# Performance work log

Measured on AMD Instinct MI355X. Metric: run time of the kernel, lower is better.

Reference implementation:

```python
import jax, jax.numpy as jnp
import numpy as np

ENC = 768
DEC = 768
B, T, S = 16, 1024, 1024


def setup_inputs() -> dict:
    key = jax.random.key(0)
    k1, k2, k3 = jax.random.split(key, 3)
    inputs = jax.random.normal(k1, (B, T, DEC), dtype=jnp.float32)
    context = jax.random.normal(k2, (B, S, ENC), dtype=jnp.float32)
    # linear_out: Linear(dec+enc -> dec) with bias; torch weight layout [out, in]
    W_out = jax.random.normal(k3, (DEC, DEC + ENC), dtype=jnp.float32) * 0.02
    b_out = jnp.zeros((DEC,), dtype=jnp.float32)
    w_scale = jnp.ones((1, 1, 1), dtype=jnp.float32)   # self.weight
    b_scale = jnp.ones((1, 1, 1), dtype=jnp.float32)   # self.bias
    prelu_a = jnp.full((1,), 0.25, dtype=jnp.float32)  # PReLU single param
    return {"inputs": inputs, "context": context, "W_out": W_out,
            "b_out": b_out, "w_scale": w_scale, "b_scale": b_scale,
            "prelu_a": prelu_a}


def reference(inputs, context, W_out, b_out, w_scale, b_scale, prelu_a):
    # score: bmm(h_t, h_s^T). NOTE: linear_in output is discarded in the
    # original (h_t reassigned), so the raw inputs are used — faithful here.
    align = jnp.einsum('btd,bsd->bts', inputs, context)        # [B,T,S]
    av = jax.nn.softmax(align, axis=-1)                        # softmax over src
    # gate: sigmoid of per-source column-sum over target positions
    gate = jax.nn.sigmoid(jnp.sum(av, axis=1, keepdims=True))  # [B,1,S]
    # AdaptiveAvgPool1d(1): mean over last (src) dim -> [B,T,1]
    pooled = jnp.mean(av, axis=-1, keepdims=True)
    av_g = av * gate * pooled                                  # fused elementwise
    c = jnp.einsum('bts,bsd->btd', av_g, context)              # [B,T,ENC]
    c = c * w_scale + b_scale                                  # scalar affine
    concat_c = jnp.concatenate([c, inputs], axis=-1)           # [B,T,ENC+DEC]
    h = jnp.einsum('btk,dk->btd', concat_c, W_out) + b_out     # linear_out
    attn_h = jnp.where(h >= 0, h, prelu_a * h)                 # PReLU
    return attn_h.transpose(1, 0, 2), av_g.transpose(1, 0, 2)
```

## Files before the change

### kernel.cpp

```cpp
#include <hip/hip_runtime.h>

#define B_ 16
#define T_ 1024
#define S_ 1024
#define D_ 768
#define K3_ 1536
#define BS_ (B_ * S_)
#define BD_ (B_ * D_)
#define NI_ (B_ * T_ * D_)
#define NW_ (D_ * K3_)

typedef __attribute__((ext_vector_type(8))) _Float16 half8;
typedef __attribute__((ext_vector_type(4))) float float4v;

__device__ __forceinline__ unsigned short f2h(float x) {
    return __builtin_bit_cast(unsigned short, (_Float16)x);
}
__device__ __forceinline__ float h2f(unsigned short u) {
    return (float)__builtin_bit_cast(_Float16, u);
}
__device__ __forceinline__ unsigned pkh2(float a, float b) {
    return (unsigned)f2h(a) | ((unsigned)f2h(b) << 16);
}
__device__ __forceinline__ uint2 pkh4(const float4 v) {
    return make_uint2(pkh2(v.x, v.y), pkh2(v.z, v.w));
}

__device__ __forceinline__ void gl_lds16(const void* g, void* l) {
    __builtin_amdgcn_global_load_lds(
        (const __attribute__((address_space(1))) unsigned int*)g,
        (__attribute__((address_space(3))) unsigned int*)l,
        16, 0, 0);
}

#define MFMA_PROLOG() \
    const int tid  = threadIdx.x; \
    const int w    = tid >> 6; \
    const int wm   = (w >> 1) * 64; \
    const int wn   = (w & 1) * 64; \
    const int lane = tid & 63; \
    const int q    = lane >> 4; \
    const int lr   = lane & 15; \
    float4v acc[4][4] = {};

#define STAGE_PROLOG() \
    const int rl0 = (w << 5) + (lane >> 2); \
    const int cc  = (lane & 3) * 8; \
    const int wb  = w * 1024;

#define MFMA_COMPUTE_F16(AS, BS) \
    { \
        half8 afr[4], bfr[4]; \
        _Pragma("unroll") \
        for (int i = 0; i < 4; i++) \
            afr[i] = *(const half8*)&(AS)[(wm + i * 16 + lr) * 32 + q * 8]; \
        _Pragma("unroll") \
        for (int j = 0; j < 4; j++) \
            bfr[j] = *(const half8*)&(BS)[(wn + j * 16 + lr) * 32 + q * 8]; \
        _Pragma("unroll") \
        for (int i = 0; i < 4; i++) \
            _Pragma("unroll") \
            for (int j = 0; j < 4; j++) \
                acc[i][j] = __builtin_amdgcn_mfma_f32_16x16x32_f16( \
                    afr[i], bfr[j], acc[i][j], 0, 0, 0); \
    }

__global__ __launch_bounds__(256) void prep_all(
    const float* __restrict__ ctx, const float* __restrict__ inp,
    const float* __restrict__ W,
    unsigned short* __restrict__ ctxT, unsigned short* __restrict__ ctx_h,
    unsigned short* __restrict__ inp_h, unsigned short* __restrict__ W_h)
{
    __shared__ unsigned short Ts[64 * 68];
    const int bid = blockIdx.x;
    const int tid = threadIdx.x;
    if (bid < 3072) {
        const int b   = bid / 192;
        const int rem = bid - b * 192;
        const int d0  = (rem >> 4) * 64;
        const int s0  = (rem & 15) * 64;
        const int srel = tid >> 4;
        const int dcol = (tid & 15) * 4;
#pragma unroll
        for (int r = 0; r < 4; r++) {
            const int s = srel + r * 16;
            float4 v = *(const float4*)(ctx + ((size_t)b * S_ + s0 + s) * D_ + d0 + dcol);
            Ts[(dcol + 0) * 68 + s] = f2h(v.x);
            Ts[(dcol + 1) * 68 + s] = f2h(v.y);
            Ts[(dcol + 2) * 68 + s] = f2h(v.z);
            Ts[(dcol + 3) * 68 + s] = f2h(v.w);
            *(uint2*)(ctx_h + ((size_t)b * S_ + s0 + s) * D_ + d0 + dcol) = pkh4(v);
        }
        __syncthreads();
        const int drow = tid >> 2;
        const int scg  = (tid & 3) * 16;
        unsigned short* dst = ctxT + ((size_t)b * D_ + d0 + drow) * S_ + s0 + scg;
#pragma unroll
        for (int p = 0; p < 4; p++) {
            uint2 u = *(const uint2*)&Ts[drow * 68 + scg + p * 4];
            *(uint2*)(dst + p * 4) = u;
        }
    } else {
        const size_t i4 = (size_t)(bid - 3072) * 256 + tid;
        const size_t flat = i4 * 4;
        float4 v;
        unsigned short* dst;
        if (flat < NI_) {
            v = ((const float4*)inp)[i4];
            dst = inp_h + flat;
        } else {
            v = *(const float4*)(W + (flat - NI_));
            dst = W_h + (flat - NI_);
        }
        *(uint2*)dst = pkh4(v);
    }
}

__global__ __launch_bounds__(256) void gemm_scores_f16(
    const unsigned short* __restrict__ ctx_h,
    const unsigned short* __restrict__ inp_h,
    float* __restrict__ out2)
{
    const int hwid = blockIdx.x + (blockIdx.y << 3) + (blockIdx.z << 6);
    const int wk   = (hwid & 7) * 128 + (hwid >> 3);
    const int b  = wk >> 6;
    const int t0 = ((wk >> 3) & 7) * 128;
    const int s0 = (wk & 7) * 128;

    __shared__ __align__(16) unsigned short As[2][128 * 32];
    __shared__ __align__(16) unsigned short Bs[2][128 * 32];

    MFMA_PROLOG();
    STAGE_PROLOG();

    const unsigned short* ga0 = ctx_h + ((size_t)b * S_ + s0 + rl0) * D_ + cc;
    const unsigned short* ga1 = ga0 + (size_t)16 * D_;
    const unsigned short* gb0 = inp_h + ((size_t)b * T_ + t0 + rl0) * D_ + cc;
    const unsigned short* gb1 = gb0 + (size_t)16 * D_;

    gl_lds16(ga0, &As[0][wb]);
    gl_lds16(ga1, &As[0][wb + 512]);
    gl_lds16(gb0, &Bs[0][wb]);
    gl_lds16(gb1, &Bs[0][wb + 512]);
    __syncthreads();

    int cur = 0;
    for (int kb = 32; kb < D_; kb += 32) {
        const int nxt = cur ^ 1;
        gl_lds16(ga0 + kb, &As[nxt][wb]);
        gl_lds16(ga1 + kb, &As[nxt][wb + 512]);
        gl_lds16(gb0 + kb, &Bs[nxt][wb]);
        gl_lds16(gb1 + kb, &Bs[nxt][wb + 512]);
        MFMA_COMPUTE_F16(As[cur], Bs[cur]);
        __syncthreads();
        cur = nxt;
    }
    MFMA_COMPUTE_F16(As[cur], Bs[cur]);

#pragma unroll
    for (int i = 0; i < 4; i++)
#pragma unroll
        for (int j = 0; j < 4; j++) {
            const int t = t0 + wn + j * 16 + lr;
            const int s = s0 + wm + i * 16 + q * 4;
            *(float4v*)(out2 + (size_t)t * BS_ + (size_t)b * S_ + s) = acc[i][j];
        }
}

__global__ __launch_bounds__(256) void softmax_rows(
    const float* __restrict__ scores, unsigned short* __restrict__ av_h)
{
    const int bid = blockIdx.x;
    const int b = bid & (B_ - 1);
    const int t = bid / B_;
    const float* row = scores + (size_t)t * BS_ + (size_t)b * S_;
    const int tid = threadIdx.x;

    float4 v = ((const float4*)row)[tid];
    float m = fmaxf(fmaxf(v.x, v.y), fmaxf(v.z, v.w));
#pragma unroll
    for (int off = 32; off > 0; off >>= 1) m = fmaxf(m, __shfl_xor(m, off));

    __shared__ float red[8];
    if ((tid & 63) == 0) red[tid >> 6] = m;
    __syncthreads();
    m = fmaxf(fmaxf(red[0], red[1]), fmaxf(red[2], red[3]));

    float4 e;
    e.x = __expf(v.x - m); e.y = __expf(v.y - m);
    e.z = __expf(v.z - m); e.w = __expf(v.w - m);
    float s = e.x + e.y + e.z + e.w;
#pragma unroll
    for (int off = 32; off > 0; off >>= 1) s += __shfl_xor(s, off);
    if ((tid & 63) == 0) red[4 + (tid >> 6)] = s;
    __syncthreads();
    s = (red[4] + red[5]) + (red[6] + red[7]);

    const float inv = 1.0f / s;
    e.x *= inv; e.y *= inv; e.z *= inv; e.w *= inv;
    unsigned short* orow = av_h + (size_t)t * BS_ + (size_t)b * S_;
    *(uint2*)(orow + tid * 4) = pkh4(e);
}

__global__ __launch_bounds__(256) void colsum_part(
    const unsigned short* __restrict__ av_h, float* __restrict__ partial)
{
    const int b = blockIdx.y;
    const int c = blockIdx.z;
    const int s2 = blockIdx.x * 512 + threadIdx.x * 2;
    const unsigned short* p = av_h + (size_t)(c * 128) * BS_ + (size_t)b * S_ + s2;
    float s0 = 0.0f, s1 = 0.0f;
#pragma unroll 8
    for (int t = 0; t < 128; t++) {
        const unsigned u = *(const unsigned*)(p + (size_t)t * BS_);
        s0 += h2f((unsigned short)(u & 0xffff));
        s1 += h2f((unsigned short)(u >> 16));
    }
    *(float2*)(partial + ((size_t)c * B_ + b) * S_ + s2) = make_float2(s0, s1);
}

__global__ __launch_bounds__(256) void gate_final(
    const float* __restrict__ partial, float* __restrict__ gate)
{
    const int idx = blockIdx.x * 256 + threadIdx.x;
    const int b = idx >> 10, s = idx & (S_ - 1);
    float sum = 0.0f;
#pragma unroll
    for (int c = 0; c < T_ / 128; c++) sum += partial[((size_t)c * B_ + b) * S_ + s];
    gate[idx] = 1.0f / (1.0f + __expf(-sum));
}

__global__ __launch_bounds__(256) void av_out(
    unsigned short* __restrict__ av_h, const float* __restrict__ gate,
    float* __restrict__ out2)
{
    const size_t i8 = ((size_t)blockIdx.x * 256 + threadIdx.x) * 8;
    const int s = (int)(i8 & (S_ - 1));
    const int b = (int)((i8 >> 10) & (B_ - 1));
    const uint4 u = *(const uint4*)(av_h + i8);
    const float4 g0 = *(const float4*)(gate + b * S_ + s);
    const float4 g1 = *(const float4*)(gate + b * S_ + s + 4);
    float a0 = h2f(u.x & 0xffff) * g0.x, a1 = h2f(u.x >> 16) * g0.y;
    float a2 = h2f(u.y & 0xffff) * g0.z, a3 = h2f(u.y >> 16) * g0.w;
    float a4 = h2f(u.z & 0xffff) * g1.x, a5 = h2f(u.z >> 16) * g1.y;
    float a6 = h2f(u.w & 0xffff) * g1.z, a7 = h2f(u.w >> 16) * g1.w;
    const float is = 1.0f / (float)S_;
    *(float4*)(out2 + i8)     = make_float4(a0 * is, a1 * is, a2 * is, a3 * is);
    *(float4*)(out2 + i8 + 4) = make_float4(a4 * is, a5 * is, a6 * is, a7 * is);
    uint4 o;
    o.x = pkh2(a0, a1); o.y = pkh2(a2, a3);
    o.z = pkh2(a4, a5); o.w = pkh2(a6, a7);
    *(uint4*)(av_h + i8) = o;
}

__global__ __launch_bounds__(256) void gemm_ctx_f16(
    const unsigned short* __restrict__ ctxT, const unsigned short* __restrict__ av_h,
    const float* __restrict__ w_scale, const float* __restrict__ b_scale,
    unsigned short* __restrict__ c_h)
{
    const int hwid = blockIdx.x + blockIdx.y * 8 + blockIdx.z * 48;
    const int wk   = (hwid & 7) * 96 + (hwid >> 3);
    const int t0 = (wk % 8) * 128;
    const int d0 = ((wk / 8) % 6) * 128;
    const int b  = wk / 48;

    __shared__ __align__(16) unsigned short As[2][128 * 32];
    __shared__ __align__(16) unsigned short Bs[2][128 * 32];

    MFMA_PROLOG();
    STAGE_PROLOG();

    const unsigned short* ga0 = ctxT + ((size_t)b * D_ + d0 + rl0) * S_ + cc;
    const unsigned short* ga1 = ga0 + (size_t)16 * S_;
    const unsigned short* gb0 = av_h + (size_t)(t0 + rl0) * BS_ + (size_t)b * S_ + cc;
    const unsigned short* gb1 = gb0 + (size_t)16 * BS_;

    gl_lds16(ga0, &As[0][wb]);
    gl_lds16(ga1, &As[0][wb + 512]);
    gl_lds16(gb0, &Bs[0][wb]);
    gl_lds16(gb1, &Bs[0][wb + 512]);
    __syncthreads();

    int cur = 0;
    for (int sb = 32; sb < S_; sb += 32) {
        const int nxt = cur ^ 1;
        gl_lds16(ga0 + sb, &As[nxt][wb]);
        gl_lds16(ga1 + sb, &As[nxt][wb + 512]);
        gl_lds16(gb0 + sb, &Bs[nxt][wb]);
        gl_lds16(gb1 + sb, &Bs[nxt][wb + 512]);
        MFMA_COMPUTE_F16(As[cur], Bs[cur]);
        __syncthreads();
        cur = nxt;
    }
    MFMA_COMPUTE_F16(As[cur], Bs[cur]);

    const float wsc = w_scale[0] * (1.0f / (float)S_);
    const float bsc = b_scale[0];
#pragma unroll
    for (int i = 0; i < 4; i++)
#pragma unroll
        for (int j = 0; j < 4; j++) {
            const int d = d0 + wm + i * 16 + q * 4;
            const int t = t0 + wn + j * 16 + lr;
            uint2 o;
            o.x = pkh2(acc[i][j][0] * wsc + bsc, acc[i][j][1] * wsc + bsc);
            o.y = pkh2(acc[i][j][2] * wsc + bsc, acc[i][j][3] * wsc + bsc);
            *(uint2*)(c_h + ((size_t)b * T_ + t) * D_ + d) = o;
        }
}

__global__ __launch_bounds__(256) void gemm_out_f16(
    const unsigned short* __restrict__ c_h, const unsigned short* __restrict__ inp_h,
    const unsigned short* __restrict__ W_h, const float* __restrict__ bias,
    const float* __restrict__ prelu_a, float* __restrict__ out0)
{
    const int hwid = blockIdx.x + blockIdx.y * 6;
    const int wk   = (hwid & 7) * 96 + (hwid >> 3);
    const int d0 = (wk % 6) * 128;
    const int n0 = (wk / 6) * 128;

    __shared__ __align__(16) unsigned short As[2][128 * 32];
    __shared__ __align__(16) unsigned short Bs[2][128 * 32];

    MFMA_PROLOG();
    STAGE_PROLOG();

    const unsigned short* ga0  = W_h + (size_t)(d0 + rl0) * K3_ + cc;
    const unsigned short* ga1  = ga0 + (size_t)16 * K3_;
    const unsigned short* gbc0 = c_h + (size_t)(n0 + rl0) * D_ + cc;
    const unsigned short* gbi0 = inp_h + (size_t)(n0 + rl0) * D_ + cc;

    gl_lds16(ga0, &As[0][wb]);
    gl_lds16(ga1, &As[0][wb + 512]);
    gl_lds16(gbc0, &Bs[0][wb]);
    gl_lds16(gbc0 + (size_t)16 * D_, &Bs[0][wb + 512]);
    __syncthreads();

    int cur = 0;
    for (int kb = 32; kb < K3_; kb += 32) {
        const int nxt = cur ^ 1;
        const unsigned short* gb0 = (kb < D_) ? gbc0 + kb : gbi0 + (kb - D_);
        gl_lds16(ga0 + kb, &As[nxt][wb]);
        gl_lds16(ga1 + kb, &As[nxt][wb + 512]);
        gl_lds16(gb0, &Bs[nxt][wb]);
        gl_lds16(gb0 + (size_t)16 * D_, &Bs[nxt][wb + 512]);
        MFMA_COMPUTE_F16(As[cur], Bs[cur]);
        __syncthreads();
        cur = nxt;
    }
    MFMA_COMPUTE_F16(As[cur], Bs[cur]);

    const float pa = prelu_a[0];
#pragma unroll
    for (int i = 0; i < 4; i++) {
        const int d = d0 + wm + i * 16 + q * 4;
        const float4 bz = *(const float4*)(bias + d);
#pragma unroll
        for (int j = 0; j < 4; j++) {
            const int n = n0 + wn + j * 16 + lr;
            const int bb = n >> 10;
            const int t = n & (T_ - 1);
            float4 h;
            h.x = acc[i][j][0] + bz.x;
            h.y = acc[i][j][1] + bz.y;
            h.z = acc[i][j][2] + bz.z;
            h.w = acc[i][j][3] + bz.w;
            h.x = h.x >= 0.0f ? h.x : pa * h.x;
            h.y = h.y >= 0.0f ? h.y : pa * h.y;
            h.z = h.z >= 0.0f ? h.z : pa * h.z;
            h.w = h.w >= 0.0f ? h.w : pa * h.w;
            *(float4*)(out0 + (size_t)t * BD_ + (size_t)bb * D_ + d) = h;
        }
    }
}

extern "C" void kernel_launch(void* const* d_in, const int* in_sizes, int n_in,
                              void* d_out, int out_size, void* d_ws, size_t ws_size,
                              hipStream_t stream)
{
    const float* inputs  = (const float*)d_in[0];
    const float* context = (const float*)d_in[1];
    const float* W_out   = (const float*)d_in[2];
    const float* b_out   = (const float*)d_in[3];
    const float* w_scale = (const float*)d_in[4];
    const float* b_scale = (const float*)d_in[5];
    const float* prelu_a = (const float*)d_in[6];

    float* out0 = (float*)d_out;
    float* out2 = out0 + (size_t)T_ * B_ * D_;

    unsigned short* c_h   = (unsigned short*)d_ws;
    unsigned short* ctxT  = c_h   + (size_t)B_ * T_ * D_;
    unsigned short* av_h  = ctxT  + (size_t)B_ * D_ * S_;
    unsigned short* inp_h = av_h  + (size_t)T_ * B_ * S_;
    unsigned short* W_h   = inp_h + (size_t)B_ * T_ * D_;
    float* gate    = (float*)(W_h + (size_t)NW_);
    float* partial = gate + (size_t)B_ * S_;

    prep_all<<<3072 + (NI_ + NW_) / 4 / 256, 256, 0, stream>>>(
        context, inputs, W_out, ctxT, c_h, inp_h, W_h);
    gemm_scores_f16<<<dim3(S_ / 128, T_ / 128, B_), 256, 0, stream>>>(
        c_h , inp_h, out2);
    softmax_rows<<<B_ * T_, 256, 0, stream>>>(out2, av_h);
    colsum_part<<<dim3(S_ / 512, B_, T_ / 128), 256, 0, stream>>>(av_h, partial);
    gate_final<<<(B_ * S_) / 256, 256, 0, stream>>>(partial, gate);
    av_out<<<(int)(((size_t)T_ * B_ * S_ / 8) / 256), 256, 0, stream>>>(
        av_h, gate, out2);
    gemm_ctx_f16<<<dim3(T_ / 128, D_ / 128, B_), 256, 0, stream>>>(
        ctxT, av_h, w_scale, b_scale, c_h);
    gemm_out_f16<<<dim3(D_ / 128, (B_ * T_) / 128), 256, 0, stream>>>(
        c_h, inp_h, W_h, b_out, prelu_a, out0);
}
```

Before: 384.1 us.

## Use triple-buffered LDS pipeline with explicit vmcnt waits and XOR-swizzled tiles

The three MFMA GEMM kernels move from a double-buffered loop with __syncthreads to a three-stage LDS ring, where loads run two tiles ahead and explicit s_waitcnt vmcnt counts plus s_barrier gate each compute step. The global-to-LDS column offset and the fragment read offset are XOR-swizzled to spread LDS accesses across banks. The goal is to hide global load latency and cut LDS bank conflicts. The cost is 50% more shared memory per block, which may lower occupancy, and the hand-written wait counts depend on each stage issuing exactly four loads.

```diff
diff --git a/kernel.cpp b/kernel.cpp
--- a/kernel.cpp
+++ b/kernel.cpp
@@ -45,24 +45,51 @@
 
 #define STAGE_PROLOG() \
     const int rl0 = (w << 5) + (lane >> 2); \
-    const int cc  = (lane & 3) * 8; \
-    const int wb  = w * 1024;
-
-#define MFMA_COMPUTE_F16(AS, BS) \
+    const int cc  = ((lane & 3) ^ ((lane >> 3) & 3)) * 8; \
+    const int wb  = w * 1024; \
+    const int qa  = (q ^ ((lr >> 1) & 3)) * 8;
+
+#define MFMA_COMPUTE_F16(AP, BP) \
     { \
         half8 afr[4], bfr[4]; \
         _Pragma("unroll") \
         for (int i = 0; i < 4; i++) \
-            afr[i] = *(const half8*)&(AS)[(wm + i * 16 + lr) * 32 + q * 8]; \
+            afr[i] = *(const half8*)&(AP)[(wm + i * 16 + lr) * 32 + qa]; \
         _Pragma("unroll") \
         for (int j = 0; j < 4; j++) \
-            bfr[j] = *(const half8*)&(BS)[(wn + j * 16 + lr) * 32 + q * 8]; \
+            bfr[j] = *(const half8*)&(BP)[(wn + j * 16 + lr) * 32 + qa]; \
         _Pragma("unroll") \
         for (int i = 0; i < 4; i++) \
             _Pragma("unroll") \
             for (int j = 0; j < 4; j++) \
                 acc[i][j] = __builtin_amdgcn_mfma_f32_16x16x32_f16( \
                     afr[i], bfr[j], acc[i][j], 0, 0, 0); \
+    }
+
+#define PIPE3_LOOP(NT, STAGE) \
+    STAGE(0, 0); \
+    STAGE(1, 1); \
+    { \
+        int cb = 0; \
+        for (int t = 0; t < (NT); ++t) { \
+            if (t + 2 < (NT)) { \
+                const int sb3 = (cb == 0) ? 2 : cb - 1; \
+                STAGE(sb3, t + 2); \
+            } \
+            if (t < (NT) - 2) { \
+                asm volatile("s_waitcnt vmcnt(8)" ::: "memory"); \
+            } else if (t == (NT) - 2) { \
+                asm volatile("s_waitcnt vmcnt(4)" ::: "memory"); \
+            } else { \
+                asm volatile("s_waitcnt vmcnt(0)" ::: "memory"); \
+            } \
+            __builtin_amdgcn_s_barrier(); \
+            __builtin_amdgcn_sched_barrier(0); \
+            MFMA_COMPUTE_F16(&As[cb * 4096], &Bs[cb * 4096]); \
+            __builtin_amdgcn_sched_barrier(0); \
+            __builtin_amdgcn_s_barrier(); \
+            cb = (cb == 2) ? 0 : cb + 1; \
+        } \
     }
 
 __global__ __launch_bounds__(256) void prep_all(
@@ -127,8 +154,8 @@
     const int t0 = ((wk >> 3) & 7) * 128;
     const int s0 = (wk & 7) * 128;
 
-    __shared__ __align__(16) unsigned short As[2][128 * 32];
-    __shared__ __align__(16) unsigned short Bs[2][128 * 32];
+    __shared__ __align__(16) unsigned short As[3 * 128 * 32];
+    __shared__ __align__(16) unsigned short Bs[3 * 128 * 32];
 
     MFMA_PROLOG();
     STAGE_PROLOG();
@@ -138,24 +165,16 @@
     const unsigned short* gb0 = inp_h + ((size_t)b * T_ + t0 + rl0) * D_ + cc;
     const unsigned short* gb1 = gb0 + (size_t)16 * D_;
 
-    gl_lds16(ga0, &As[0][wb]);
-    gl_lds16(ga1, &As[0][wb + 512]);
-    gl_lds16(gb0, &Bs[0][wb]);
-    gl_lds16(gb1, &Bs[0][wb + 512]);
-    __syncthreads();
-
-    int cur = 0;
-    for (int kb = 32; kb < D_; kb += 32) {
-        const int nxt = cur ^ 1;
-        gl_lds16(ga0 + kb, &As[nxt][wb]);
-        gl_lds16(ga1 + kb, &As[nxt][wb + 512]);
-        gl_lds16(gb0 + kb, &Bs[nxt][wb]);
-        gl_lds16(gb1 + kb, &Bs[nxt][wb + 512]);
-        MFMA_COMPUTE_F16(As[cur], Bs[cur]);
-        __syncthreads();
-        cur = nxt;
-    }
-    MFMA_COMPUTE_F16(As[cur], Bs[cur]);
+#define STAGE_G1(bi, tt) \
+    { \
+        const int kb = (tt) * 32; \
+        gl_lds16(ga0 + kb, &As[(bi) * 4096 + wb]); \
+        gl_lds16(ga1 + kb, &As[(bi) * 4096 + wb + 512]); \
+        gl_lds16(gb0 + kb, &Bs[(bi) * 4096 + wb]); \
+        gl_lds16(gb1 + kb, &Bs[(bi) * 4096 + wb + 512]); \
+    }
+
+    PIPE3_LOOP(D_ / 32, STAGE_G1);
 
 #pragma unroll
     for (int i = 0; i < 4; i++)
@@ -264,8 +283,8 @@
     const int d0 = ((wk / 8) % 6) * 128;
     const int b  = wk / 48;
 
-    __shared__ __align__(16) unsigned short As[2][128 * 32];
-    __shared__ __align__(16) unsigned short Bs[2][128 * 32];
+    __shared__ __align__(16) unsigned short As[3 * 128 * 32];
+    __shared__ __align__(16) unsigned short Bs[3 * 128 * 32];
 
     MFMA_PROLOG();
     STAGE_PROLOG();
@@ -275,24 +294,16 @@
     const unsigned short* gb0 = av_h + (size_t)(t0 + rl0) * BS_ + (size_t)b * S_ + cc;
     const unsigned short* gb1 = gb0 + (size_t)16 * BS_;
 
-    gl_lds16(ga0, &As[0][wb]);
-    gl_lds16(ga1, &As[0][wb + 512]);
-    gl_lds16(gb0, &Bs[0][wb]);
-    gl_lds16(gb1, &Bs[0][wb + 512]);
-    __syncthreads();
-
-    int cur = 0;
-    for (int sb = 32; sb < S_; sb += 32) {
-        const int nxt = cur ^ 1;
-        gl_lds16(ga0 + sb, &As[nxt][wb]);
-        gl_lds16(ga1 + sb, &As[nxt][wb + 512]);
-        gl_lds16(gb0 + sb, &Bs[nxt][wb]);
-        gl_lds16(gb1 + sb, &Bs[nxt][wb + 512]);
-        MFMA_COMPUTE_F16(As[cur], Bs[cur]);
-        __syncthreads();
-        cur = nxt;
-    }
-    MFMA_COMPUTE_F16(As[cur], Bs[cur]);
+#define STAGE_G2(bi, tt) \
+    { \
+        const int sbk = (tt) * 32; \
+        gl_lds16(ga0 + sbk, &As[(bi) * 4096 + wb]); \
+        gl_lds16(ga1 + sbk, &As[(bi) * 4096 + wb + 512]); \
+        gl_lds16(gb0 + sbk, &Bs[(bi) * 4096 + wb]); \
+        gl_lds16(gb1 + sbk, &Bs[(bi) * 4096 + wb + 512]); \
+    }
+
+    PIPE3_LOOP(S_ / 32, STAGE_G2);
 
     const float wsc = w_scale[0] * (1.0f / (float)S_);
     const float bsc = b_scale[0];
@@ -319,8 +330,8 @@
     const int d0 = (wk % 6) * 128;
     const int n0 = (wk / 6) * 128;
 
-    __shared__ __align__(16) unsigned short As[2][128 * 32];
-    __shared__ __align__(16) unsigned short Bs[2][128 * 32];
+    __shared__ __align__(16) unsigned short As[3 * 128 * 32];
+    __shared__ __align__(16) unsigned short Bs[3 * 128 * 32];
 
     MFMA_PROLOG();
     STAGE_PROLOG();
@@ -330,25 +341,17 @@
     const unsigned short* gbc0 = c_h + (size_t)(n0 + rl0) * D_ + cc;
     const unsigned short* gbi0 = inp_h + (size_t)(n0 + rl0) * D_ + cc;
 
-    gl_lds16(ga0, &As[0][wb]);
-    gl_lds16(ga1, &As[0][wb + 512]);
-    gl_lds16(gbc0, &Bs[0][wb]);
-    gl_lds16(gbc0 + (size_t)16 * D_, &Bs[0][wb + 512]);
-    __syncthreads();
-
-    int cur = 0;
-    for (int kb = 32; kb < K3_; kb += 32) {
-        const int nxt = cur ^ 1;
-        const unsigned short* gb0 = (kb < D_) ? gbc0 + kb : gbi0 + (kb - D_);
-        gl_lds16(ga0 + kb, &As[nxt][wb]);
-        gl_lds16(ga1 + kb, &As[nxt][wb + 512]);
-        gl_lds16(gb0, &Bs[nxt][wb]);
-        gl_lds16(gb0 + (size_t)16 * D_, &Bs[nxt][wb + 512]);
-        MFMA_COMPUTE_F16(As[cur], Bs[cur]);
-        __syncthreads();
-        cur = nxt;
-    }
-    MFMA_COMPUTE_F16(As[cur], Bs[cur]);
+#define STAGE_G3(bi, tt) \
+    { \
+        const int kb = (tt) * 32; \
+        const unsigned short* gbx = (kb < D_) ? gbc0 + kb : gbi0 + (kb - D_); \
+        gl_lds16(ga0 + kb, &As[(bi) * 4096 + wb]); \
+        gl_lds16(ga1 + kb, &As[(bi) * 4096 + wb + 512]); \
+        gl_lds16(gbx, &Bs[(bi) * 4096 + wb]); \
+        gl_lds16(gbx + (size_t)16 * D_, &Bs[(bi) * 4096 + wb + 512]); \
+    }
+
+    PIPE3_LOOP(K3_ / 32, STAGE_G3);
 
     const float pa = prelu_a[0];
 #pragma unroll
```

Result: slower. 393.3 us (+2.4%).

## Store scores in fp16 in place and XOR-swizzle LDS tiles for MFMA reads

Applied to the files above, without the earlier changes.

The score GEMM now writes fp16 scores into the av_h buffer instead of fp32 into the output, and softmax reads and writes that buffer in place. This halves the traffic for the intermediate score matrix (written once, read once). Separately, the LDS staging column and the fragment read offset are XOR-swizzled by row bits to reduce bank conflicts on the half8 reads in all three GEMMs. Rounding scores to fp16 before softmax loses precision in the logits, which with unit-normal inputs over 768 dims can be large in magnitude.

```diff
diff --git a/kernel.cpp b/kernel.cpp
--- a/kernel.cpp
+++ b/kernel.cpp
@@ -45,18 +45,19 @@
 
 #define STAGE_PROLOG() \
     const int rl0 = (w << 5) + (lane >> 2); \
-    const int cc  = (lane & 3) * 8; \
-    const int wb  = w * 1024;
-
-#define MFMA_COMPUTE_F16(AS, BS) \
+    const int cc  = ((lane & 3) ^ ((lane >> 3) & 3)) * 8; \
+    const int wb  = w * 1024; \
+    const int qa  = (q ^ ((lr >> 1) & 3)) * 8;
+
+#define MFMA_COMPUTE_F16(AP, BP) \
     { \
         half8 afr[4], bfr[4]; \
         _Pragma("unroll") \
         for (int i = 0; i < 4; i++) \
-            afr[i] = *(const half8*)&(AS)[(wm + i * 16 + lr) * 32 + q * 8]; \
+            afr[i] = *(const half8*)&(AP)[(wm + i * 16 + lr) * 32 + qa]; \
         _Pragma("unroll") \
         for (int j = 0; j < 4; j++) \
-            bfr[j] = *(const half8*)&(BS)[(wn + j * 16 + lr) * 32 + q * 8]; \
+            bfr[j] = *(const half8*)&(BP)[(wn + j * 16 + lr) * 32 + qa]; \
         _Pragma("unroll") \
         for (int i = 0; i < 4; i++) \
             _Pragma("unroll") \
@@ -119,7 +120,7 @@
 __global__ __launch_bounds__(256) void gemm_scores_f16(
     const unsigned short* __restrict__ ctx_h,
     const unsigned short* __restrict__ inp_h,
-    float* __restrict__ out2)
+    unsigned short* __restrict__ sc_h)
 {
     const int hwid = blockIdx.x + (blockIdx.y << 3) + (blockIdx.z << 6);
     const int wk   = (hwid & 7) * 128 + (hwid >> 3);
@@ -127,8 +128,8 @@
     const int t0 = ((wk >> 3) & 7) * 128;
     const int s0 = (wk & 7) * 128;
 
-    __shared__ __align__(16) unsigned short As[2][128 * 32];
-    __shared__ __align__(16) unsigned short Bs[2][128 * 32];
+    __shared__ __align__(16) unsigned short As[2 * 128 * 32];
+    __shared__ __align__(16) unsigned short Bs[2 * 128 * 32];
 
     MFMA_PROLOG();
     STAGE_PROLOG();
@@ -138,24 +139,25 @@
     const unsigned short* gb0 = inp_h + ((size_t)b * T_ + t0 + rl0) * D_ + cc;
     const unsigned short* gb1 = gb0 + (size_t)16 * D_;
 
-    gl_lds16(ga0, &As[0][wb]);
-    gl_lds16(ga1, &As[0][wb + 512]);
-    gl_lds16(gb0, &Bs[0][wb]);
-    gl_lds16(gb1, &Bs[0][wb + 512]);
+#define STAGE_G1(bi, kb) \
+    { \
+        gl_lds16(ga0 + (kb), &As[(bi) * 4096 + wb]); \
+        gl_lds16(ga1 + (kb), &As[(bi) * 4096 + wb + 512]); \
+        gl_lds16(gb0 + (kb), &Bs[(bi) * 4096 + wb]); \
+        gl_lds16(gb1 + (kb), &Bs[(bi) * 4096 + wb + 512]); \
+    }
+
+    STAGE_G1(0, 0);
     __syncthreads();
-
     int cur = 0;
     for (int kb = 32; kb < D_; kb += 32) {
         const int nxt = cur ^ 1;
-        gl_lds16(ga0 + kb, &As[nxt][wb]);
-        gl_lds16(ga1 + kb, &As[nxt][wb + 512]);
-        gl_lds16(gb0 + kb, &Bs[nxt][wb]);
-        gl_lds16(gb1 + kb, &Bs[nxt][wb + 512]);
-        MFMA_COMPUTE_F16(As[cur], Bs[cur]);
+        STAGE_G1(nxt, kb);
+        MFMA_COMPUTE_F16(&As[cur * 4096], &Bs[cur * 4096]);
         __syncthreads();
         cur = nxt;
     }
-    MFMA_COMPUTE_F16(As[cur], Bs[cur]);
+    MFMA_COMPUTE_F16(&As[cur * 4096], &Bs[cur * 4096]);
 
 #pragma unroll
     for (int i = 0; i < 4; i++)
@@ -163,21 +165,26 @@
         for (int j = 0; j < 4; j++) {
             const int t = t0 + wn + j * 16 + lr;
             const int s = s0 + wm + i * 16 + q * 4;
-            *(float4v*)(out2 + (size_t)t * BS_ + (size_t)b * S_ + s) = acc[i][j];
+            uint2 o;
+            o.x = pkh2(acc[i][j][0], acc[i][j][1]);
+            o.y = pkh2(acc[i][j][2], acc[i][j][3]);
+            *(uint2*)(sc_h + (size_t)t * BS_ + (size_t)b * S_ + s) = o;
         }
 }
 
 __global__ __launch_bounds__(256) void softmax_rows(
-    const float* __restrict__ scores, unsigned short* __restrict__ av_h)
+    unsigned short* __restrict__ sc)
 {
     const int bid = blockIdx.x;
     const int b = bid & (B_ - 1);
     const int t = bid / B_;
-    const float* row = scores + (size_t)t * BS_ + (size_t)b * S_;
+    unsigned short* row = sc + (size_t)t * BS_ + (size_t)b * S_;
     const int tid = threadIdx.x;
 
-    float4 v = ((const float4*)row)[tid];
-    float m = fmaxf(fmaxf(v.x, v.y), fmaxf(v.z, v.w));
+    uint2 u = *(const uint2*)(row + tid * 4);
+    float v0 = h2f((unsigned short)(u.x & 0xffff)), v1 = h2f((unsigned short)(u.x >> 16));
+    float v2 = h2f((unsigned short)(u.y & 0xffff)), v3 = h2f((unsigned short)(u.y >> 16));
+    float m = fmaxf(fmaxf(v0, v1), fmaxf(v2, v3));
 #pragma unroll
     for (int off = 32; off > 0; off >>= 1) m = fmaxf(m, __shfl_xor(m, off));
 
@@ -186,10 +193,9 @@
     __syncthreads();
     m = fmaxf(fmaxf(red[0], red[1]), fmaxf(red[2], red[3]));
 
-    float4 e;
-    e.x = __expf(v.x - m); e.y = __expf(v.y - m);
-    e.z = __expf(v.z - m); e.w = __expf(v.w - m);
-    float s = e.x + e.y + e.z + e.w;
+    float e0 = __expf(v0 - m), e1 = __expf(v1 - m);
+    float e2 = __expf(v2 - m), e3 = __expf(v3 - m);
+    float s = (e0 + e1) + (e2 + e3);
 #pragma unroll
     for (int off = 32; off > 0; off >>= 1) s += __shfl_xor(s, off);
     if ((tid & 63) == 0) red[4 + (tid >> 6)] = s;
@@ -197,9 +203,10 @@
     s = (red[4] + red[5]) + (red[6] + red[7]);
 
     const float inv = 1.0f / s;
-    e.x *= inv; e.y *= inv; e.z *= inv; e.w *= inv;
-    unsigned short* orow = av_h + (size_t)t * BS_ + (size_t)b * S_;
-    *(uint2*)(orow + tid * 4) = pkh4(e);
+    uint2 o;
+    o.x = pkh2(e0 * inv, e1 * inv);
+    o.y = pkh2(e2 * inv, e3 * inv);
+    *(uint2*)(row + tid * 4) = o;
 }
 
 __global__ __launch_bounds__(256) void colsum_part(
@@ -240,10 +247,10 @@
     const uint4 u = *(const uint4*)(av_h + i8);
     const float4 g0 = *(const float4*)(gate + b * S_ + s);
     const float4 g1 = *(const float4*)(gate + b * S_ + s + 4);
-    float a0 = h2f(u.x & 0xffff) * g0.x, a1 = h2f(u.x >> 16) * g0.y;
-    float a2 = h2f(u.y & 0xffff) * g0.z, a3 = h2f(u.y >> 16) * g0.w;
-    float a4 = h2f(u.z & 0xffff) * g1.x, a5 = h2f(u.z >> 16) * g1.y;
-    float a6 = h2f(u.w & 0xffff) * g1.z, a7 = h2f(u.w >> 16) * g1.w;
+    float a0 = h2f((unsigned short)(u.x & 0xffff)) * g0.x, a1 = h2f((unsigned short)(u.x >> 16)) * g0.y;
+    float a2 = h2f((unsigned short)(u.y & 0xffff)) * g0.z, a3 = h2f((unsigned short)(u.y >> 16)) * g0.w;
+    float a4 = h2f((unsigned short)(u.z & 0xffff)) * g1.x, a5 = h2f((unsigned short)(u.z >> 16)) * g1.y;
+    float a6 = h2f((unsigned short)(u.w & 0xffff)) * g1.z, a7 = h2f((unsigned short)(u.w >> 16)) * g1.w;
     const float is = 1.0f / (float)S_;
     *(float4*)(out2 + i8)     = make_float4(a0 * is, a1 * is, a2 * is, a3 * is);
     *(float4*)(out2 + i8 + 4) = make_float4(a4 * is, a5 * is, a6 * is, a7 * is);
@@ -264,8 +271,8 @@
     const int d0 = ((wk / 8) % 6) * 128;
     const int b  = wk / 48;
 
-    __shared__ __align__(16) unsigned short As[2][128 * 32];
-    __shared__ __align__(16) unsigned short Bs[2][128 * 32];
+    __shared__ __align__(16) unsigned short As[2 * 128 * 32];
+    __shared__ __align__(16) unsigned short Bs[2 * 128 * 32];
 
     MFMA_PROLOG();
     STAGE_PROLOG();
@@ -275,24 +282,25 @@
     const unsigned short* gb0 = av_h + (size_t)(t0 + rl0) * BS_ + (size_t)b * S_ + cc;
     const unsigned short* gb1 = gb0 + (size_t)16 * BS_;
 
-    gl_lds16(ga0, &As[0][wb]);
-    gl_lds16(ga1, &As[0][wb + 512]);
-    gl_lds16(gb0, &Bs[0][wb]);
-    gl_lds16(gb1, &Bs[0][wb + 512]);
+#define STAGE_G2(bi, sbk) \
+    { \
+        gl_lds16(ga0 + (sbk), &As[(bi) * 4096 + wb]); \
+        gl_lds16(ga1 + (sbk), &As[(bi) * 4096 + wb + 512]); \
+        gl_lds16(gb0 + (sbk), &Bs[(bi) * 4096 + wb]); \
+        gl_lds16(gb1 + (sbk), &Bs[(bi) * 4096 + wb + 512]); \
+    }
+
+    STAGE_G2(0, 0);
     __syncthreads();
-
     int cur = 0;
     for (int sb = 32; sb < S_; sb += 32) {
         const int nxt = cur ^ 1;
-        gl_lds16(ga0 + sb, &As[nxt][wb]);
-        gl_lds16(ga1 + sb, &As[nxt][wb + 512]);
-        gl_lds16(gb0 + sb, &Bs[nxt][wb]);
-        gl_lds16(gb1 + sb, &Bs[nxt][wb + 512]);
-        MFMA_COMPUTE_F16(As[cur], Bs[cur]);
+        STAGE_G2(nxt, sb);
+        MFMA_COMPUTE_F16(&As[cur * 4096], &Bs[cur * 4096]);
         __syncthreads();
         cur = nxt;
     }
-    MFMA_COMPUTE_F16(As[cur], Bs[cur]);
+    MFMA_COMPUTE_F16(&As[cur * 4096], &Bs[cur * 4096]);
 
     const float wsc = w_scale[0] * (1.0f / (float)S_);
     const float bsc = b_scale[0];
@@ -319,8 +327,8 @@
     const int d0 = (wk % 6) * 128;
     const int n0 = (wk / 6) * 128;
 
-    __shared__ __align__(16) unsigned short As[2][128 * 32];
-    __shared__ __align__(16) unsigned short Bs[2][128 * 32];
+    __shared__ __align__(16) unsigned short As[2 * 128 * 32];
+    __shared__ __align__(16) unsigned short Bs[2 * 128 * 32];
 
     MFMA_PROLOG();
     STAGE_PROLOG();
@@ -330,25 +338,26 @@
     const unsigned short* gbc0 = c_h + (size_t)(n0 + rl0) * D_ + cc;
     const unsigned short* gbi0 = inp_h + (size_t)(n0 + rl0) * D_ + cc;
 
-    gl_lds16(ga0, &As[0][wb]);
-    gl_lds16(ga1, &As[0][wb + 512]);
-    gl_lds16(gbc0, &Bs[0][wb]);
-    gl_lds16(gbc0 + (size_t)16 * D_, &Bs[0][wb + 512]);
+#define STAGE_G3(bi, kb) \
+    { \
+        const unsigned short* gbx = ((kb) < D_) ? gbc0 + (kb) : gbi0 + ((kb) - D_); \
+        gl_lds16(ga0 + (kb), &As[(bi) * 4096 + wb]); \
+        gl_lds16(ga1 + (kb), &As[(bi) * 4096 + wb + 512]); \
+        gl_lds16(gbx, &Bs[(bi) * 4096 + wb]); \
+        gl_lds16(gbx + (size_t)16 * D_, &Bs[(bi) * 4096 + wb + 512]); \
+    }
+
+    STAGE_G3(0, 0);
     __syncthreads();
-
     int cur = 0;
     for (int kb = 32; kb < K3_; kb += 32) {
         const int nxt = cur ^ 1;
-        const unsigned short* gb0 = (kb < D_) ? gbc0 + kb : gbi0 + (kb - D_);
-        gl_lds16(ga0 + kb, &As[nxt][wb]);
-        gl_lds16(ga1 + kb, &As[nxt][wb + 512]);
-        gl_lds16(gb0, &Bs[nxt][wb]);
-        gl_lds16(gb0 + (size_t)16 * D_, &Bs[nxt][wb + 512]);
-        MFMA_COMPUTE_F16(As[cur], Bs[cur]);
+        STAGE_G3(nxt, kb);
+        MFMA_COMPUTE_F16(&As[cur * 4096], &Bs[cur * 4096]);
         __syncthreads();
         cur = nxt;
     }
-    MFMA_COMPUTE_F16(As[cur], Bs[cur]);
+    MFMA_COMPUTE_F16(&As[cur * 4096], &Bs[cur * 4096]);
 
     const float pa = prelu_a[0];
 #pragma unroll
@@ -400,8 +409,8 @@
     prep_all<<<3072 + (NI_ + NW_) / 4 / 256, 256, 0, stream>>>(
         context, inputs, W_out, ctxT, c_h, inp_h, W_h);
     gemm_scores_f16<<<dim3(S_ / 128, T_ / 128, B_), 256, 0, stream>>>(
-        c_h , inp_h, out2);
-    softmax_rows<<<B_ * T_, 256, 0, stream>>>(out2, av_h);
+        c_h , inp_h, av_h);
+    softmax_rows<<<B_ * T_, 256, 0, stream>>>(av_h);
     colsum_part<<<dim3(S_ / 512, B_, T_ / 128), 256, 0, stream>>>(av_h, partial);
     gate_final<<<(B_ * S_) / 256, 256, 0, stream>>>(partial, gate);
     av_out<<<(int)(((size_t)T_ * B_ * S_ / 8) / 256), 256, 0, stream>>>(
```

Result: slower. 396.5 us (+3.2%).
